# Optimization experiments

Measured on AMD Instinct MI355X. Metric: run time of the kernel, lower is better.

The kernel has to match this reference:

```python
import jax, jax.numpy as jnp
import numpy as np

B, V, W, H = 512, 256, 64, 64  # batch, num_variables, window, hidden_size


def setup_inputs() -> dict:
    key = jax.random.key(0)
    ks = jax.random.split(key, 10)
    s = 0.05
    return {
        "x": jax.random.normal(ks[0], (B, V, W), dtype=jnp.float32),
        # nn.LSTM(input=V, hidden=H): gate order i, f, g, o
        "w_ih": jax.random.normal(ks[1], (4 * H, V), dtype=jnp.float32) * s,
        "w_hh": jax.random.normal(ks[2], (4 * H, H), dtype=jnp.float32) * s,
        "b_ih": jax.random.normal(ks[3], (4 * H,), dtype=jnp.float32) * s,
        "b_hh": jax.random.normal(ks[4], (4 * H,), dtype=jnp.float32) * s,
        # linear_v: Linear(window, 1, bias=False)
        "w_v": jax.random.normal(ks[5], (1, W), dtype=jnp.float32) * s,
        # linear_w: Linear(2H, window)
        "w_w": jax.random.normal(ks[6], (W, 2 * H), dtype=jnp.float32) * s,
        "b_w": jax.random.normal(ks[7], (W,), dtype=jnp.float32) * s,
        # linear_u: Linear(window, window)
        "w_u": jax.random.normal(ks[8], (W, W), dtype=jnp.float32) * s,
        "b_u": jax.random.normal(ks[9], (W,), dtype=jnp.float32) * s,
    }


def reference(x, w_ih, w_hh, b_ih, b_hh, w_v, w_w, b_w, w_u, b_u):
    batch, n_var, window = x.shape
    hidden = w_hh.shape[1]
    # linear_u over the window (last) dim: (B, V, W)
    u_out = jnp.einsum("bvw,uw->bvu", x, w_u) + b_u
    x_steps = jnp.transpose(x, (2, 0, 1))  # (W, B, V)

    def step(carry, x_t):
        h, c = carry  # each (B, H)
        # input attention
        wout = jnp.concatenate([h, c], axis=1) @ w_w.T + b_w          # (B, W)
        score = jnp.einsum("bvw,w->bv", jnp.tanh(wout[:, None, :] + u_out), w_v[0])
        alpha = jax.nn.softmax(score, axis=1)                          # (B, V)
        x_tilde = alpha * x_t                                          # (B, V)
        # LSTM cell (torch gate order i, f, g, o)
        gates = x_tilde @ w_ih.T + b_ih + h @ w_hh.T + b_hh            # (B, 4H)
        i_g, f_g, g_g, o_g = jnp.split(gates, 4, axis=1)
        i_g = jax.nn.sigmoid(i_g)
        f_g = jax.nn.sigmoid(f_g)
        g_g = jnp.tanh(g_g)
        o_g = jax.nn.sigmoid(o_g)
        c_new = f_g * c + i_g * g_g
        h_new = o_g * jnp.tanh(c_new)
        return (h_new, c_new), (x_tilde, h_new)

    init = (jnp.zeros((batch, hidden), x.dtype), jnp.zeros((batch, hidden), x.dtype))
    _, (x_tilde_seq, h_seq) = jax.lax.scan(step, init, x_steps)
    # matches torch.stack(x_tilde_list) (W,B,V) and torch.stack(h_list) (W,B,H)
    return x_tilde_seq, h_seq
```

## Files before the change

### kernel.cpp

```cpp
#include <hip/hip_runtime.h>


#define KLOG2E  1.4426950408889634f
#define K2LOG2E 2.8853900817779268f

typedef _Float16 h2    __attribute__((ext_vector_type(2)));
typedef __fp16   f16x8 __attribute__((ext_vector_type(8)));
typedef float    f32x4 __attribute__((ext_vector_type(4)));
union H2U { h2 h; unsigned u; };

__device__ __forceinline__ float frcp(float x)  { return __builtin_amdgcn_rcpf(x); }
__device__ __forceinline__ float fexp2(float x) { return __builtin_amdgcn_exp2f(x); }
__device__ __forceinline__ float fsigmoid(float x) { return frcp(1.f + fexp2(-KLOG2E * x)); }
__device__ __forceinline__ float ftanh(float x) { return 1.f - 2.f * frcp(fexp2(K2LOG2E * x) + 1.f); }

__device__ __forceinline__ unsigned pkrtz_u(float a, float b) {
    H2U r; r.h = __builtin_bit_cast(h2, __builtin_amdgcn_cvt_pkrtz(a, b)); return r.u;
}

#define L_EA   0
#define L_EB   17408
#define L_PSA  34816
#define L_PSB  35328
#define L_XTA  35840
#define L_XTB  36096
#define L_XHA  36352
#define L_XHB  36480
#define L_EWA  36608
#define L_EWB  36672
#define L_HCA  36736
#define L_HCB  36864
#define L_HHA  36992
#define L_HHB  37024
#define L_BI   37056
#define L_WV   37312
#define L_TOT  37376

__global__ __launch_bounds__(512, 2) void enc_kernel(
    const float* __restrict__ x,
    const float* __restrict__ w_ih,
    const float* __restrict__ w_hh,
    const float* __restrict__ b_ih,
    const float* __restrict__ b_hh,
    const float* __restrict__ w_v,
    const float* __restrict__ w_w,
    const float* __restrict__ b_w,
    const float* __restrict__ w_u,
    const float* __restrict__ b_u,
    float* __restrict__ out_xt,
    float* __restrict__ out_h)
{
    extern __shared__ float lds[];
    float*    EA   = lds + L_EA;    float*    EB   = lds + L_EB;
    float*    psA  = lds + L_PSA;   float*    psB  = lds + L_PSB;
    float*    xtA  = lds + L_XTA;   float*    xtB  = lds + L_XTB;
    unsigned* xhA  = (unsigned*)(lds + L_XHA);
    unsigned* xhB  = (unsigned*)(lds + L_XHB);
    float*    ewA  = lds + L_EWA;   float*    ewB  = lds + L_EWB;
    float*    hcA  = lds + L_HCA;   float*    hcB  = lds + L_HCB;
    unsigned* hhA  = (unsigned*)(lds + L_HHA);
    unsigned* hhB  = (unsigned*)(lds + L_HHB);
    float*    biasL= lds + L_BI;
    float*    wv2L = lds + L_WV;

    const int tid  = threadIdx.x;
    const int lane = tid & 63;
    const int wvi  = tid >> 6;
    const int bA   = blockIdx.x;
    const int bB   = blockIdx.x + 256;

    f16x8 wbx0[8], wbx1[8], wbh0[2], wbh1[2];
    {
        const int col0 = wvi*32 + (lane & 15);
        const int col1 = col0 + 16;
        const int kofs = (lane >> 4) * 8;
#pragma unroll
        for (int kk = 0; kk < 8; ++kk) {
            const float* s0 = w_ih + col0*256 + kk*32 + kofs;
            const float* s1 = w_ih + col1*256 + kk*32 + kofs;
            f16x8 a, b;
#pragma unroll
            for (int i = 0; i < 8; ++i) { a[i] = (__fp16)s0[i]; b[i] = (__fp16)s1[i]; }
            wbx0[kk] = a; wbx1[kk] = b;
        }
#pragma unroll
        for (int kk = 0; kk < 2; ++kk) {
            const float* s0 = w_hh + col0*64 + kk*32 + kofs;
            const float* s1 = w_hh + col1*64 + kk*32 + kofs;
            f16x8 a, b;
#pragma unroll
            for (int i = 0; i < 8; ++i) { a[i] = (__fp16)s0[i]; b[i] = (__fp16)s1[i]; }
            wbh0[kk] = a; wbh1[kk] = b;
        }
    }
    const int w8 = wvi*8 + (lane & 7);
    const int kg = lane >> 3;
    float4 www4[4];
#pragma unroll
    for (int m = 0; m < 4; ++m)
        www4[m] = *(const float4*)&w_w[w8*128 + kg*4 + 32*m];
    const float bwr = b_w[w8];
    float Sv = 0.f;
#pragma unroll
    for (int wi = 0; wi < 64; ++wi) Sv += w_v[wi];
    const float bu_lane = b_u[lane];

    if (tid < 256) biasL[tid] = b_ih[tid] + b_hh[tid];
    if (tid < 64) wv2L[tid] = -2.f * w_v[tid];
    if (tid < 128) { hcA[tid] = 0.f; hcB[tid] = 0.f; }
    if (tid < 32)  { hhA[tid] = 0u; hhB[tid] = 0u; }

#pragma unroll 1
    for (int bb = 0; bb < 2; ++bb) {
        float* E = bb ? EB : EA;
        const int b = bb ? bB : bA;
#pragma unroll 1
        for (int half = 0; half < 2; ++half) {
            float4 wu_r[8];
#pragma unroll
            for (int i = 0; i < 8; ++i)
                wu_r[i] = *(const float4*)&w_u[lane*64 + half*32 + 4*i];
            const float* xb = x + b*16384 + half*32;
#pragma unroll 2
            for (int vi = 0; vi < 32; ++vi) {
                int v = __builtin_amdgcn_readfirstlane(wvi*32 + vi);
                const float4* xr = (const float4*)(xb + v*64);
                float acc = 0.f;
#pragma unroll
                for (int i = 0; i < 8; ++i) {
                    float4 xx = xr[i]; float4 wu = wu_r[i];
                    acc += xx.x*wu.x + xx.y*wu.y + xx.z*wu.z + xx.w*wu.w;
                }
                if (half == 0) E[v*68 + lane] = acc + bu_lane;
                else           E[v*68 + lane] = fexp2(K2LOG2E * (E[v*68 + lane] + acc));
            }
        }
    }
    __syncthreads();

    const int  xj   = tid & 255;
    const int  bsel = tid >> 8;
    const float* xrow = x + (bsel ? bB : bA)*16384 + xj*64;
    const float* Erow = (bsel ? EB : EA) + xj*68;
    const float* ewX  = bsel ? ewB : ewA;
    float*       psX  = bsel ? psB : psA;
    float xcur = xrow[0];

    for (int t = 0; t < 64; ++t) {
        {
            float accA = 0.f, accB = 0.f;
#pragma unroll
            for (int m = 0; m < 4; ++m) {
                float4 w4 = www4[m];
                float4 hA = *(const float4*)&hcA[kg*4 + 32*m];
                float4 hB = *(const float4*)&hcB[kg*4 + 32*m];
                accA += hA.x*w4.x + hA.y*w4.y + hA.z*w4.z + hA.w*w4.w;
                accB += hB.x*w4.x + hB.y*w4.y + hB.z*w4.z + hB.w*w4.w;
            }
#pragma unroll
            for (int off = 8; off <= 32; off <<= 1) {
                accA += __shfl_xor(accA, off, 64);
                accB += __shfl_xor(accB, off, 64);
            }
            if (kg == 0)      ewA[w8] = fexp2(K2LOG2E * (accA + bwr));
            else if (kg == 1) ewB[w8] = fexp2(K2LOG2E * (accB + bwr));
        }
        float xnxt = (t < 63) ? xrow[t + 1] : 0.f;
        __syncthreads();

        {
            float ac0 = 0.f, ac1 = 0.f, ac2 = 0.f, ac3 = 0.f;
#pragma unroll
            for (int q = 0; q < 16; ++q) {
                float4 e4 = *(const float4*)&Erow[4*q];
                float4 c4 = *(const float4*)&ewX[4*q];
                float4 v4 = *(const float4*)&wv2L[4*q];
                ac0 += v4.x * frcp(e4.x*c4.x + 1.f);
                ac1 += v4.y * frcp(e4.y*c4.y + 1.f);
                ac2 += v4.z * frcp(e4.z*c4.z + 1.f);
                ac3 += v4.w * frcp(e4.w*c4.w + 1.f);
            }
            float acc = Sv + ((ac0 + ac1) + (ac2 + ac3));
            float e  = fexp2(KLOG2E * acc);
            psX[xj]       = e;
            psX[256 + xj] = e * xcur;
        }
        xcur = xnxt;
        __syncthreads();

        if (wvi < 2) {
            float*    ps = wvi ? psB : psA;
            float*    xt = wvi ? xtB : xtA;
            unsigned* xh = wvi ? xhB : xhA;
            float4 ev = *(const float4*)&ps[4*lane];
            float4 ex = *(const float4*)&ps[256 + 4*lane];
            float sum = (ev.x + ev.y) + (ev.z + ev.w);
#pragma unroll
            for (int off = 1; off <= 32; off <<= 1) sum += __shfl_xor(sum, off, 64);
            float r = frcp(sum);
            float4 xo;
            xo.x = ex.x*r; xo.y = ex.y*r; xo.z = ex.z*r; xo.w = ex.w*r;
            *(float4*)&xt[4*lane] = xo;
            xh[2*lane]     = pkrtz_u(xo.x, xo.y);
            xh[2*lane + 1] = pkrtz_u(xo.z, xo.w);
        }
        __syncthreads();

        {
            float xtv = bsel ? xtB[xj] : xtA[xj];
            out_xt[t*131072 + (bsel ? bB : bA)*256 + xj] = xtv;

            const int row = lane & 15;
            const int q4  = (lane >> 4) * 4;
            f32x4 ax0 = {0.f,0.f,0.f,0.f}, ax1 = {0.f,0.f,0.f,0.f};
            f32x4 ah0 = {0.f,0.f,0.f,0.f}, ah1 = {0.f,0.f,0.f,0.f};
            const unsigned* xsrc = (row == 1) ? xhB : xhA;
#pragma unroll
            for (int kk = 0; kk < 8; ++kk) {
                f16x8 a = {};
                if (row < 2)
                    a = __builtin_bit_cast(f16x8, *(const uint4*)(xsrc + kk*16 + q4));
                ax0 = __builtin_amdgcn_mfma_f32_16x16x32_f16(a, wbx0[kk], ax0, 0, 0, 0);
                ax1 = __builtin_amdgcn_mfma_f32_16x16x32_f16(a, wbx1[kk], ax1, 0, 0, 0);
            }
            const unsigned* hsrc = (row == 1) ? hhB : hhA;
#pragma unroll
            for (int kk = 0; kk < 2; ++kk) {
                f16x8 a = {};
                if (row < 2)
                    a = __builtin_bit_cast(f16x8, *(const uint4*)(hsrc + kk*16 + q4));
                ah0 = __builtin_amdgcn_mfma_f32_16x16x32_f16(a, wbh0[kk], ah0, 0, 0, 0);
                ah1 = __builtin_amdgcn_mfma_f32_16x16x32_f16(a, wbh1[kk], ah1, 0, 0, 0);
            }
            if (lane < 16) {
                const int j0 = wvi*32 + lane, j1 = j0 + 16;
                psA[j0] = ax0[0] + ah0[0];
                psA[j1] = ax1[0] + ah1[0];
                psB[j0] = ax0[1] + ah0[1];
                psB[j1] = ax1[1] + ah1[1];
            }
        }
        __syncthreads();

        if (wvi < 2) {
            float*    ps = wvi ? psB : psA;
            float*    hc = wvi ? hcB : hcA;
            unsigned* hh = wvi ? hhB : hhA;
            float*    oh = out_h + t*32768 + (wvi ? bB : bA)*64;
            const int k = lane;
            float gi = fsigmoid(biasL[k      ] + ps[k      ]);
            float gf = fsigmoid(biasL[64  + k] + ps[64  + k]);
            float gg = ftanh   (biasL[128 + k] + ps[128 + k]);
            float go = fsigmoid(biasL[192 + k] + ps[192 + k]);
            float cn = gf * hc[64 + k] + gi * gg;
            float hn = go * ftanh(cn);
            hc[k] = hn; hc[64 + k] = cn;
            float hp = __shfl_xor(hn, 1, 64);
            if (!(lane & 1)) hh[k >> 1] = pkrtz_u(hn, hp);
            oh[k] = hn;
        }
        __syncthreads();
    }
}

extern "C" void kernel_launch(void* const* d_in, const int* in_sizes, int n_in,
                              void* d_out, int out_size, void* d_ws, size_t ws_size,
                              hipStream_t stream) {
    const float* x    = (const float*)d_in[0];
    const float* w_ih = (const float*)d_in[1];
    const float* w_hh = (const float*)d_in[2];
    const float* b_ih = (const float*)d_in[3];
    const float* b_hh = (const float*)d_in[4];
    const float* w_v  = (const float*)d_in[5];
    const float* w_w  = (const float*)d_in[6];
    const float* b_w  = (const float*)d_in[7];
    const float* w_u  = (const float*)d_in[8];
    const float* b_u  = (const float*)d_in[9];

    float* out_xt = (float*)d_out;
    float* out_h  = out_xt + 64*512*256;

    const size_t shbytes = (size_t)L_TOT * sizeof(float);
    (void)hipFuncSetAttribute((const void*)enc_kernel,
                        hipFuncAttributeMaxDynamicSharedMemorySize, (int)shbytes);
    enc_kernel<<<dim3(256), dim3(512), shbytes, stream>>>(
        x, w_ih, w_hh, b_ih, b_hh, w_v, w_w, b_w, w_u, b_u, out_xt, out_h);
}
```

Baseline: 281.6 us.

## Defer softmax normalization past input GEMM and drop a barrier stage

```diff
diff --git a/kernel.cpp b/kernel.cpp
--- a/kernel.cpp
+++ b/kernel.cpp
@@ -21,20 +21,19 @@
 #define L_EA   0
 #define L_EB   17408
 #define L_PSA  34816
-#define L_PSB  35328
-#define L_XTA  35840
-#define L_XTB  36096
-#define L_XHA  36352
-#define L_XHB  36480
-#define L_EWA  36608
-#define L_EWB  36672
-#define L_HCA  36736
-#define L_HCB  36864
-#define L_HHA  36992
-#define L_HHB  37024
-#define L_BI   37056
-#define L_WV   37312
-#define L_TOT  37376
+#define L_PSB  35072
+#define L_XHA  35328
+#define L_XHB  35456
+#define L_EWA  35584
+#define L_EWB  35648
+#define L_HCA  35712
+#define L_HCB  35840
+#define L_HHA  35968
+#define L_HHB  36000
+#define L_BI   36032
+#define L_WV   36288
+#define L_WS   36352
+#define L_TOT  36360
 
 __global__ __launch_bounds__(512, 2) void enc_kernel(
     const float* __restrict__ x,
@@ -53,7 +52,6 @@
     extern __shared__ float lds[];
     float*    EA   = lds + L_EA;    float*    EB   = lds + L_EB;
     float*    psA  = lds + L_PSA;   float*    psB  = lds + L_PSB;
-    float*    xtA  = lds + L_XTA;   float*    xtB  = lds + L_XTB;
     unsigned* xhA  = (unsigned*)(lds + L_XHA);
     unsigned* xhB  = (unsigned*)(lds + L_XHB);
     float*    ewA  = lds + L_EWA;   float*    ewB  = lds + L_EWB;
@@ -62,6 +60,7 @@
     unsigned* hhB  = (unsigned*)(lds + L_HHB);
     float*    biasL= lds + L_BI;
     float*    wv2L = lds + L_WV;
+    float*    wsum = lds + L_WS;
 
     const int tid  = threadIdx.x;
     const int lane = tid & 63;
@@ -143,10 +142,14 @@
     const float* xrow = x + (bsel ? bB : bA)*16384 + xj*64;
     const float* Erow = (bsel ? EB : EA) + xj*68;
     const float* ewX  = bsel ? ewB : ewA;
-    float*       psX  = bsel ? psB : psA;
+    unsigned*    xhX  = bsel ? xhB : xhA;
     float xcur = xrow[0];
 
+    const int mrow = lane & 15;
+    const int q4   = (lane >> 4) * 4;
+
     for (int t = 0; t < 64; ++t) {
+        f32x4 ah0 = {0.f,0.f,0.f,0.f}, ah1 = {0.f,0.f,0.f,0.f};
         {
             float accA = 0.f, accB = 0.f;
 #pragma unroll
@@ -157,6 +160,15 @@
                 accA += hA.x*w4.x + hA.y*w4.y + hA.z*w4.z + hA.w*w4.w;
                 accB += hB.x*w4.x + hB.y*w4.y + hB.z*w4.z + hB.w*w4.w;
             }
+            const unsigned* hsrc = (mrow == 1) ? hhB : hhA;
+#pragma unroll
+            for (int kk = 0; kk < 2; ++kk) {
+                f16x8 a = {};
+                if (mrow < 2)
+                    a = __builtin_bit_cast(f16x8, *(const uint4*)(hsrc + kk*16 + q4));
+                ah0 = __builtin_amdgcn_mfma_f32_16x16x32_f16(a, wbh0[kk], ah0, 0, 0, 0);
+                ah1 = __builtin_amdgcn_mfma_f32_16x16x32_f16(a, wbh1[kk], ah1, 0, 0, 0);
+            }
 #pragma unroll
             for (int off = 8; off <= 32; off <<= 1) {
                 accA += __shfl_xor(accA, off, 64);
@@ -168,6 +180,7 @@
         float xnxt = (t < 63) ? xrow[t + 1] : 0.f;
         __syncthreads();
 
+        float exreg;
         {
             float ac0 = 0.f, ac1 = 0.f, ac2 = 0.f, ac3 = 0.f;
 #pragma unroll
@@ -182,62 +195,38 @@
             }
             float acc = Sv + ((ac0 + ac1) + (ac2 + ac3));
             float e  = fexp2(KLOG2E * acc);
-            psX[xj]       = e;
-            psX[256 + xj] = e * xcur;
+            exreg = e * xcur;
+            float s = e;
+#pragma unroll
+            for (int off = 1; off <= 32; off <<= 1) s += __shfl_xor(s, off, 64);
+            if (lane == 0) wsum[wvi] = s;
+            float ex2 = __shfl_xor(exreg, 1, 64);
+            if (!(lane & 1)) xhX[xj >> 1] = pkrtz_u(exreg, ex2);
         }
         xcur = xnxt;
         __syncthreads();
 
-        if (wvi < 2) {
-            float*    ps = wvi ? psB : psA;
-            float*    xt = wvi ? xtB : xtA;
-            unsigned* xh = wvi ? xhB : xhA;
-            float4 ev = *(const float4*)&ps[4*lane];
-            float4 ex = *(const float4*)&ps[256 + 4*lane];
-            float sum = (ev.x + ev.y) + (ev.z + ev.w);
-#pragma unroll
-            for (int off = 1; off <= 32; off <<= 1) sum += __shfl_xor(sum, off, 64);
-            float r = frcp(sum);
-            float4 xo;
-            xo.x = ex.x*r; xo.y = ex.y*r; xo.z = ex.z*r; xo.w = ex.w*r;
-            *(float4*)&xt[4*lane] = xo;
-            xh[2*lane]     = pkrtz_u(xo.x, xo.y);
-            xh[2*lane + 1] = pkrtz_u(xo.z, xo.w);
-        }
-        __syncthreads();
-
         {
-            float xtv = bsel ? xtB[xj] : xtA[xj];
-            out_xt[t*131072 + (bsel ? bB : bA)*256 + xj] = xtv;
-
-            const int row = lane & 15;
-            const int q4  = (lane >> 4) * 4;
+            float rA = frcp((wsum[0] + wsum[1]) + (wsum[2] + wsum[3]));
+            float rB = frcp((wsum[4] + wsum[5]) + (wsum[6] + wsum[7]));
+            out_xt[t*131072 + (bsel ? bB : bA)*256 + xj] = (bsel ? rB : rA) * exreg;
+
             f32x4 ax0 = {0.f,0.f,0.f,0.f}, ax1 = {0.f,0.f,0.f,0.f};
-            f32x4 ah0 = {0.f,0.f,0.f,0.f}, ah1 = {0.f,0.f,0.f,0.f};
-            const unsigned* xsrc = (row == 1) ? xhB : xhA;
+            const unsigned* xsrc = (mrow == 1) ? xhB : xhA;
 #pragma unroll
             for (int kk = 0; kk < 8; ++kk) {
                 f16x8 a = {};
-                if (row < 2)
+                if (mrow < 2)
                     a = __builtin_bit_cast(f16x8, *(const uint4*)(xsrc + kk*16 + q4));
                 ax0 = __builtin_amdgcn_mfma_f32_16x16x32_f16(a, wbx0[kk], ax0, 0, 0, 0);
                 ax1 = __builtin_amdgcn_mfma_f32_16x16x32_f16(a, wbx1[kk], ax1, 0, 0, 0);
             }
-            const unsigned* hsrc = (row == 1) ? hhB : hhA;
-#pragma unroll
-            for (int kk = 0; kk < 2; ++kk) {
-                f16x8 a = {};
-                if (row < 2)
-                    a = __builtin_bit_cast(f16x8, *(const uint4*)(hsrc + kk*16 + q4));
-                ah0 = __builtin_amdgcn_mfma_f32_16x16x32_f16(a, wbh0[kk], ah0, 0, 0, 0);
-                ah1 = __builtin_amdgcn_mfma_f32_16x16x32_f16(a, wbh1[kk], ah1, 0, 0, 0);
-            }
             if (lane < 16) {
                 const int j0 = wvi*32 + lane, j1 = j0 + 16;
-                psA[j0] = ax0[0] + ah0[0];
-                psA[j1] = ax1[0] + ah1[0];
-                psB[j0] = ax0[1] + ah0[1];
-                psB[j1] = ax1[1] + ah1[1];
+                psA[j0] = rA*ax0[0] + ah0[0];
+                psA[j1] = rA*ax1[0] + ah1[0];
+                psB[j0] = rB*ax0[1] + ah0[1];
+                psB[j1] = rB*ax1[1] + ah1[1];
             }
         }
         __syncthreads();
```

Measured after the change: 284.1 us. About the same (+0.9%).
